# Performance work log

Hardware: AMD Instinct MI355X
Metric: run time of the kernel (lower is better)

Reference implementation:

```python
import jax, jax.numpy as jnp
import numpy as np

WEIGHT_BITS = 8
INPUT_BITS = 8


def fake_quant(t, bits):
    """Per-tensor symmetric absmax fake quantization with straight-through estimator."""
    qmax = 2.0 ** (bits - 1) - 1.0  # e.g. 127 for 8 bits
    scale = jnp.maximum(jnp.max(jnp.abs(t)), 1e-8) / qmax
    q = jnp.round(t / scale) * scale
    return t + jax.lax.stop_gradient(q - t)


def setup_inputs() -> dict:
    key = jax.random.key(0)
    k0, k1, k2, k3 = jax.random.split(key, 4)
    d, f, n = 4096, 11008, 4096
    s_in = 1.0 / np.sqrt(d)
    s_ff = 1.0 / np.sqrt(f)
    return {
        "x": jax.random.normal(k0, (n, d), jnp.float32),
        "w1": jax.random.normal(k1, (f, d), jnp.float32) * s_in,  # fc1: embed -> ffn
        "w3": jax.random.normal(k2, (f, d), jnp.float32) * s_in,  # fc3: gate proj
        "w2": jax.random.normal(k3, (d, f), jnp.float32) * s_ff,  # fc2: ffn -> embed
    }


def reference(x, w1, w3, w2):
    # quantized fc3 -> silu gate
    xq = fake_quant(x, INPUT_BITS)
    gate = jax.nn.silu(jnp.einsum('nd,fd->nf', xq, fake_quant(w3, WEIGHT_BITS)))
    # quantized fc1, multiplied by gate (GLU)
    h = jnp.einsum('nd,fd->nf', xq, fake_quant(w1, WEIGHT_BITS)) * gate
    # subln=False -> no ffn_layernorm; dropout=0 (eval)
    hq = fake_quant(h, INPUT_BITS)
    out = jnp.einsum('nf,df->nd', hq, fake_quant(w2, WEIGHT_BITS))
    return out
```

## Files before the change

### kernel.cpp

```cpp
#include <hip/hip_runtime.h>
#include <hip/hip_bf16.h>

typedef __attribute__((ext_vector_type(4))) int int4v;

#define MFMA_I8(a, b, c) __builtin_amdgcn_mfma_i32_16x16x64_i8((a), (b), (c), 0, 0, 0)
#define GLDS16(g, l)                                                                        \
  __builtin_amdgcn_global_load_lds((const __attribute__((address_space(1))) void*)(g),      \
                                   (__attribute__((address_space(3))) void*)(l), 16, 0, 0)
#define SBAR() __builtin_amdgcn_s_barrier()
#define SCHED0() __builtin_amdgcn_sched_barrier(0)

static constexpr int NTOK = 4096;
static constexpr int DDIM = 4096;
static constexpr int FDIM = 11008;


__device__ __forceinline__ float wave_max64(float m) {
#pragma unroll
  for (int o = 32; o > 0; o >>= 1) m = fmaxf(m, __shfl_xor(m, o));
  return m;
}

__global__ void zero_slots(unsigned* s) {
  if (threadIdx.x < 16) s[threadIdx.x] = 0u;
}

__device__ __forceinline__ void absmax_body(const float* __restrict__ p, int n4,
                                            unsigned* __restrict__ slot) {
  float m = 0.f;
  const int stride = gridDim.x * blockDim.x;
  for (int i = blockIdx.x * blockDim.x + threadIdx.x; i < n4; i += stride) {
    float4 v = reinterpret_cast<const float4*>(p)[i];
    m = fmaxf(fmaxf(fabsf(v.x), fabsf(v.y)), fmaxf(fmaxf(fabsf(v.z), fabsf(v.w)), m));
  }
  m = wave_max64(m);
  __shared__ float wm[4];
  const int lane = threadIdx.x & 63, w = threadIdx.x >> 6;
  if (lane == 0) wm[w] = m;
  __syncthreads();
  if (threadIdx.x == 0) {
    m = fmaxf(fmaxf(wm[0], wm[1]), fmaxf(wm[2], wm[3]));
    atomicMax(slot, __float_as_uint(m));
  }
}

__global__ void absmax4(const float* x, const float* w1, const float* w3, const float* w2,
                        unsigned* slots, int n4x, int n4w) {
  const int seg = blockIdx.y;
  const float* p = (seg == 0) ? x : (seg == 1) ? w1 : (seg == 2) ? w3 : w2;
  absmax_body(p, seg == 0 ? n4x : n4w, slots + seg);
}

__device__ __forceinline__ void quant_body(const float* __restrict__ in,
                                           unsigned* __restrict__ out, int n4,
                                           const unsigned* __restrict__ slot) {
  const float s = fmaxf(__uint_as_float(*slot), 1e-8f) / 127.0f;
  const int stride = gridDim.x * blockDim.x;
  for (int i = blockIdx.x * blockDim.x + threadIdx.x; i < n4; i += stride) {
    float4 v = reinterpret_cast<const float4*>(in)[i];
    const int q0 = (int)rintf(v.x / s), q1 = (int)rintf(v.y / s);
    const int q2 = (int)rintf(v.z / s), q3 = (int)rintf(v.w / s);
    out[i] = (unsigned)(q0 & 255) | ((unsigned)(q1 & 255) << 8) |
             ((unsigned)(q2 & 255) << 16) | ((unsigned)(q3 & 255) << 24);
  }
}

__device__ __forceinline__ void quantW_frag_body(const float* __restrict__ in,
                                                 int4v* __restrict__ out,
                                                 const unsigned* __restrict__ slot,
                                                 int K, int NKT, int total) {
  const float s = fmaxf(__uint_as_float(*slot), 1e-8f) / 127.0f;
  const int stride = gridDim.x * blockDim.x;
  for (int u = blockIdx.x * blockDim.x + threadIdx.x; u < total; u += stride) {
    const int block = u >> 8;
    const int sidx = u & 255;
    const int fi = sidx >> 6;
    const int l = sidx & 63;
    const int p = block / NKT;
    const int kt = block - p * NKT;
    const int row = p * 32 + (fi & 1) * 16 + (l & 15);
    const int k0 = kt * 128 + (fi >> 1) * 64 + (l >> 4) * 16;
    const float4* src = reinterpret_cast<const float4*>(in + (size_t)row * K + k0);
    unsigned r[4];
#pragma unroll
    for (int j = 0; j < 4; ++j) {
      float4 v = src[j];
      const int q0 = (int)rintf(v.x / s), q1 = (int)rintf(v.y / s);
      const int q2 = (int)rintf(v.z / s), q3 = (int)rintf(v.w / s);
      r[j] = (unsigned)(q0 & 255) | ((unsigned)(q1 & 255) << 8) |
             ((unsigned)(q2 & 255) << 16) | ((unsigned)(q3 & 255) << 24);
    }
    out[u] = (int4v){(int)r[0], (int)r[1], (int)r[2], (int)r[3]};
  }
}

__global__ void quant4(const float* x, const float* w1, const float* w3, const float* w2,
                       unsigned* qx, unsigned* qw1, unsigned* qw3, unsigned* qw2,
                       const unsigned* slots, int n4x, int n4w) {
  const int seg = blockIdx.y;
  const int totW = FDIM * (DDIM / 16);
  if (seg == 0) quant_body(x, qx, n4x, slots + 0);
  else if (seg == 1) quantW_frag_body(w1, (int4v*)qw1, slots + 1, DDIM, DDIM / 128, totW);
  else if (seg == 2) quantW_frag_body(w3, (int4v*)qw3, slots + 2, DDIM, DDIM / 128, totW);
  else quant_body(w2, qw2, n4w, slots + 3);
}

__global__ void quant_kernel(const float* __restrict__ in, unsigned* __restrict__ out,
                             int n4, const unsigned* __restrict__ slot) {
  quant_body(in, out, n4, slot);
}

__global__ __launch_bounds__(256, 2) void gemm_glu(
    const signed char* __restrict__ Aq, const signed char* __restrict__ B3f,
    const signed char* __restrict__ B1f, float* __restrict__ H,
    const unsigned* __restrict__ slots, unsigned* __restrict__ hslot) {
  constexpr int K = DDIM;
  constexpr int NT = K >> 7;
  __shared__ char lds[32768];

  const int t = threadIdx.x;
  const int l = t & 63;
  const int w = t >> 6;

  const int gx = gridDim.x, gy = gridDim.y;
  const int nwg = gx * gy;
  const int i0 = blockIdx.y * gx + blockIdx.x;
  const int cid = (i0 & 7) * (nwg >> 3) + (i0 >> 3);
  const int rowA0 = (cid % gy) << 7;
  const int colB0 = (cid / gy) << 7;

  const int rlA = t >> 3;
  const int glA = (t & 7) ^ (rlA & 7);
  const signed char* aP = Aq + (size_t)(rowA0 + rlA) * K + glA * 16;
  const size_t r32 = (size_t)32 * K;
  const int stW = w * 1024;

  const int p0 = (colB0 >> 5) + w;
  const signed char* w3b = B3f + (size_t)p0 * 32 * 4096 + l * 16;
  const signed char* w1b = B1f + (size_t)p0 * 32 * 4096 + l * 16;

#define STAGE_A(KT, BUF)                                   \
  do {                                                     \
    const size_t kO_ = (size_t)(KT) * 128;                 \
    GLDS16(aP + kO_, &lds[(BUF) + stW]);                   \
    GLDS16(aP + r32 + kO_, &lds[(BUF) + 4096 + stW]);      \
    GLDS16(aP + 2 * r32 + kO_, &lds[(BUF) + 8192 + stW]);  \
    GLDS16(aP + 3 * r32 + kO_, &lds[(BUF) + 12288 + stW]); \
  } while (0)

#define LDSF(BASE, R, G)                                                      \
  (*reinterpret_cast<const int4v*>(                                           \
      &lds[(BASE) + (R)*128 + (((G) ^ ((R)&7)) << 4)]))

  int4v acc3[8][2], acc1[8][2];
#pragma unroll
  for (int m = 0; m < 8; ++m)
#pragma unroll
    for (int n = 0; n < 2; ++n) {
      acc3[m][n] = (int4v){0, 0, 0, 0};
      acc1[m][n] = (int4v){0, 0, 0, 0};
    }

  const int lr = l & 15;
  const int cr = l >> 4;

  int4v b3k0[2], b3k1[2], b1k0[2], b1k1[2];

  STAGE_A(0, 0);
  {
    b3k0[0] = *(const int4v*)(w3b);
    b3k0[1] = *(const int4v*)(w3b + 1024);
    b3k1[0] = *(const int4v*)(w3b + 2048);
    b3k1[1] = *(const int4v*)(w3b + 3072);
    b1k0[0] = *(const int4v*)(w1b);
    b1k0[1] = *(const int4v*)(w1b + 1024);
    b1k1[0] = *(const int4v*)(w1b + 2048);
    b1k1[1] = *(const int4v*)(w1b + 3072);
  }

  for (int kt = 0; kt < NT; ++kt) {
    const int rb = (kt & 1) * 16384;
    const bool nx = (kt + 1 < NT);
    const signed char* p3n = w3b + (size_t)(kt + 1) * 4096;
    const signed char* p1n = w1b + (size_t)(kt + 1) * 4096;

    SCHED0();
    asm volatile("s_waitcnt vmcnt(8)" ::: "memory");
    SBAR();
    SCHED0();

    if (nx) STAGE_A(kt + 1, rb ^ 16384);

    int4v a_[8];
#pragma unroll
    for (int m = 0; m < 8; ++m) a_[m] = LDSF(rb, m * 16 + lr, cr);
    __builtin_amdgcn_s_setprio(1);
#pragma unroll
    for (int m = 0; m < 8; ++m) {
      acc3[m][0] = MFMA_I8(a_[m], b3k0[0], acc3[m][0]);
      acc3[m][1] = MFMA_I8(a_[m], b3k0[1], acc3[m][1]);
      acc1[m][0] = MFMA_I8(a_[m], b1k0[0], acc1[m][0]);
      acc1[m][1] = MFMA_I8(a_[m], b1k0[1], acc1[m][1]);
    }
    __builtin_amdgcn_s_setprio(0);

    if (nx) {
      b3k0[0] = *(const int4v*)(p3n);
      b3k0[1] = *(const int4v*)(p3n + 1024);
      b1k0[0] = *(const int4v*)(p1n);
      b1k0[1] = *(const int4v*)(p1n + 1024);
    }

#pragma unroll
    for (int m = 0; m < 8; ++m) a_[m] = LDSF(rb, m * 16 + lr, 4 + cr);
    __builtin_amdgcn_s_setprio(1);
#pragma unroll
    for (int m = 0; m < 8; ++m) {
      acc3[m][0] = MFMA_I8(a_[m], b3k1[0], acc3[m][0]);
      acc3[m][1] = MFMA_I8(a_[m], b3k1[1], acc3[m][1]);
      acc1[m][0] = MFMA_I8(a_[m], b1k1[0], acc1[m][0]);
      acc1[m][1] = MFMA_I8(a_[m], b1k1[1], acc1[m][1]);
    }
    __builtin_amdgcn_s_setprio(0);

    if (nx) {
      b3k1[0] = *(const int4v*)(p3n + 2048);
      b3k1[1] = *(const int4v*)(p3n + 3072);
      b1k1[0] = *(const int4v*)(p1n + 2048);
      b1k1[1] = *(const int4v*)(p1n + 3072);
    }
  }

  const float sx = fmaxf(__uint_as_float(slots[0]), 1e-8f) / 127.0f;
  const float sw1 = fmaxf(__uint_as_float(slots[1]), 1e-8f) / 127.0f;
  const float sw3 = fmaxf(__uint_as_float(slots[2]), 1e-8f) / 127.0f;
  const float s3 = sx * sw3, s1 = sx * sw1;
  const int crow0 = rowA0 + ((l >> 4) << 2);
  const int ccol0 = colB0 + w * 32 + lr;
  float hmax = 0.f;
#pragma unroll
  for (int m = 0; m < 8; ++m)
#pragma unroll
    for (int n = 0; n < 2; ++n)
#pragma unroll
      for (int j = 0; j < 4; ++j) {
        const int row = crow0 + m * 16 + j;
        const int col = ccol0 + n * 16;
        const float g = (float)acc3[m][n][j] * s3;
        const float gate = g / (1.f + expf(-g));
        const float h = (float)acc1[m][n][j] * s1 * gate;
        H[(size_t)row * FDIM + col] = h;
        hmax = fmaxf(hmax, fabsf(h));
      }
  hmax = wave_max64(hmax);
  if (l == 0) atomicMax(hslot, __float_as_uint(hmax));
#undef STAGE_A
#undef LDSF
}

__global__ __launch_bounds__(512, 2) void gemm_down(
    const signed char* __restrict__ Aq, const signed char* __restrict__ Bq,
    float* __restrict__ C, const unsigned* __restrict__ slots, int sA, int sB,
    int K, int ldc) {
  __shared__ char lds[131072];

  const int t = threadIdx.x;
  const int l = t & 63;
  const int w = t >> 6;
  const int wm = w >> 2;
  const int wn = w & 3;

  const int gx = gridDim.x, gy = gridDim.y;
  const int nwg = gx * gy;
  const int i0 = blockIdx.y * gx + blockIdx.x;
  const int cid = (i0 & 7) * (nwg >> 3) + (i0 >> 3);
  const int rowA0 = (cid % gy) << 8;
  const int colB0 = (cid / gy) << 8;

  const int rl = t >> 3;
  const int gl = (t & 7) ^ (rl & 7);
  const signed char* aP = Aq + (size_t)(rowA0 + rl) * K + gl * 16;
  const signed char* bP = Bq + (size_t)(colB0 + rl) * K + gl * 16;
  const size_t r64 = (size_t)64 * K;
  const int stW = w * 1024;

#define STAGE8(KO, BASE)                                             \
  do {                                                               \
    GLDS16(aP + (KO), &lds[(BASE) + stW]);                           \
    GLDS16(aP + r64 + (KO), &lds[(BASE) + 8192 + stW]);              \
    GLDS16(aP + 2 * r64 + (KO), &lds[(BASE) + 16384 + stW]);         \
    GLDS16(aP + 3 * r64 + (KO), &lds[(BASE) + 24576 + stW]);         \
    GLDS16(bP + (KO), &lds[(BASE) + 32768 + stW]);                   \
    GLDS16(bP + r64 + (KO), &lds[(BASE) + 40960 + stW]);             \
    GLDS16(bP + 2 * r64 + (KO), &lds[(BASE) + 49152 + stW]);         \
    GLDS16(bP + 3 * r64 + (KO), &lds[(BASE) + 57344 + stW]);         \
  } while (0)

#define LDSF(BASE, ROW, G)                                                    \
  (*reinterpret_cast<const int4v*>(                                           \
      &lds[(BASE) + (ROW)*128 + (((G) ^ ((ROW)&7)) << 4)]))

  int4v acc[8][4];
#pragma unroll
  for (int m = 0; m < 8; ++m)
#pragma unroll
    for (int n = 0; n < 4; ++n) acc[m][n] = (int4v){0, 0, 0, 0};

  const int NT = K >> 7;
  const int arow = wm * 128 + (l & 15);
  const int brow = wn * 64 + (l & 15);
  const int cr = l >> 4;

  STAGE8(0, 0);

  for (int kt = 0; kt < NT; ++kt) {
    const int rb = (kt & 1) * 65536;
    SCHED0();
    asm volatile("s_waitcnt vmcnt(0)" ::: "memory");
    SBAR();
    SCHED0();

    if (kt + 1 < NT) STAGE8((size_t)(kt + 1) * 128, rb ^ 65536);

#pragma unroll
    for (int kk = 0; kk < 2; ++kk) {
      int4v a[8], b[4];
#pragma unroll
      for (int m = 0; m < 8; ++m) a[m] = LDSF(rb, arow + m * 16, kk * 4 + cr);
#pragma unroll
      for (int n = 0; n < 4; ++n) b[n] = LDSF(rb + 32768, brow + n * 16, kk * 4 + cr);
      __builtin_amdgcn_s_setprio(1);
#pragma unroll
      for (int m = 0; m < 8; ++m)
#pragma unroll
        for (int n = 0; n < 4; ++n) acc[m][n] = MFMA_I8(a[m], b[n], acc[m][n]);
      __builtin_amdgcn_s_setprio(0);
    }
  }

  const float sa = fmaxf(__uint_as_float(slots[sA]), 1e-8f) / 127.0f;
  const float sb2 = fmaxf(__uint_as_float(slots[sB]), 1e-8f) / 127.0f;
  const float s = sa * sb2;
  const int crow0 = rowA0 + wm * 128 + ((l >> 4) << 2);
  const int ccol0 = colB0 + wn * 64 + (l & 15);
#pragma unroll
  for (int m = 0; m < 8; ++m)
#pragma unroll
    for (int n = 0; n < 4; ++n)
#pragma unroll
      for (int j = 0; j < 4; ++j) {
        const int row = crow0 + m * 16 + j;
        const int col = ccol0 + n * 16;
        C[(size_t)row * ldc + col] = (float)acc[m][n][j] * s;
      }
#undef STAGE8
#undef LDSF
}


extern "C" void kernel_launch(void* const* d_in, const int* in_sizes, int n_in,
                              void* d_out, int out_size, void* d_ws, size_t ws_size,
                              hipStream_t stream) {
  const float* x = (const float*)d_in[0];
  const float* w1 = (const float*)d_in[1];
  const float* w3 = (const float*)d_in[2];
  const float* w2 = (const float*)d_in[3];
  float* out = (float*)d_out;
  char* ws = (char*)d_ws;

  unsigned* slots = (unsigned*)ws;
  size_t off = 256;
  signed char* qx = (signed char*)(ws + off);
  off += (size_t)NTOK * DDIM;
  signed char* qw3 = (signed char*)(ws + off);
  off += (size_t)FDIM * DDIM;
  signed char* qw1 = (signed char*)(ws + off);
  off += (size_t)FDIM * DDIM;
  signed char* qw2 = (signed char*)(ws + off);
  off += (size_t)FDIM * DDIM;
  float* H = (float*)(ws + off);
  off += (size_t)NTOK * FDIM * 4;
  signed char* qh = (signed char*)(ws + off);
  off += (size_t)NTOK * FDIM;

  const int n4x = NTOK * DDIM / 4;
  const int n4w = FDIM * DDIM / 4;
  const int n4h = NTOK * FDIM / 4;

  zero_slots<<<1, 64, 0, stream>>>(slots);
  absmax4<<<dim3(512, 4), 256, 0, stream>>>(x, w1, w3, w2, slots, n4x, n4w);
  quant4<<<dim3(2048, 4), 256, 0, stream>>>(x, w1, w3, w2, (unsigned*)qx, (unsigned*)qw1,
                                            (unsigned*)qw3, (unsigned*)qw2, slots, n4x, n4w);

  const dim3 gGlu(FDIM / 128, NTOK / 128);
  gemm_glu<<<gGlu, 256, 0, stream>>>(qx, qw3, qw1, H, slots, slots + 4);
  quant_kernel<<<2048, 256, 0, stream>>>(H, (unsigned*)qh, n4h, slots + 4);
  const dim3 gDn(DDIM / 256, NTOK / 256);
  gemm_down<<<gDn, 512, 0, stream>>>(qh, qw2, out, slots, 4, 3, FDIM, DDIM);
}
```

Before: 819.0 us.

## Double K-tile depth in GLU GEMM and replace slot-zero kernel with memset

The GLU GEMM now stages 256-wide K tiles of A into a 64KB double-buffered LDS (previously 128-wide in 32KB). It prefetches four k-steps of B fragments into registers and processes the M dimension in two halves, which halves the number of barriers and loop iterations. This adds LDS usage that may cut the two-blocks-per-CU occupancy and raises register pressure from the larger B prefetch. The zero_slots launch is also replaced by hipMemsetAsync.

```diff
diff --git a/kernel.cpp b/kernel.cpp
--- a/kernel.cpp
+++ b/kernel.cpp
@@ -19,10 +19,6 @@
 #pragma unroll
   for (int o = 32; o > 0; o >>= 1) m = fmaxf(m, __shfl_xor(m, o));
   return m;
-}
-
-__global__ void zero_slots(unsigned* s) {
-  if (threadIdx.x < 16) s[threadIdx.x] = 0u;
 }
 
 __device__ __forceinline__ void absmax_body(const float* __restrict__ p, int n4,
@@ -115,8 +111,8 @@
     const signed char* __restrict__ B1f, float* __restrict__ H,
     const unsigned* __restrict__ slots, unsigned* __restrict__ hslot) {
   constexpr int K = DDIM;
-  constexpr int NT = K >> 7;
-  __shared__ char lds[32768];
+  constexpr int NT = K >> 8;
+  __shared__ char lds[65536];
 
   const int t = threadIdx.x;
   const int l = t & 63;
@@ -129,28 +125,32 @@
   const int rowA0 = (cid % gy) << 7;
   const int colB0 = (cid / gy) << 7;
 
-  const int rlA = t >> 3;
-  const int glA = (t & 7) ^ (rlA & 7);
+  const int rlA = t >> 4;
+  const int glA = (t & 15) ^ (rlA & 7);
   const signed char* aP = Aq + (size_t)(rowA0 + rlA) * K + glA * 16;
-  const size_t r32 = (size_t)32 * K;
+  const size_t r16 = (size_t)16 * K;
   const int stW = w * 1024;
 
   const int p0 = (colB0 >> 5) + w;
   const signed char* w3b = B3f + (size_t)p0 * 32 * 4096 + l * 16;
   const signed char* w1b = B1f + (size_t)p0 * 32 * 4096 + l * 16;
 
-#define STAGE_A(KT, BUF)                                   \
-  do {                                                     \
-    const size_t kO_ = (size_t)(KT) * 128;                 \
-    GLDS16(aP + kO_, &lds[(BUF) + stW]);                   \
-    GLDS16(aP + r32 + kO_, &lds[(BUF) + 4096 + stW]);      \
-    GLDS16(aP + 2 * r32 + kO_, &lds[(BUF) + 8192 + stW]);  \
-    GLDS16(aP + 3 * r32 + kO_, &lds[(BUF) + 12288 + stW]); \
+#define STAGE_A(KT, BUF)                                              \
+  do {                                                                \
+    const size_t kO_ = (size_t)(KT) * 256;                            \
+    GLDS16(aP + kO_, &lds[(BUF) + stW]);                              \
+    GLDS16(aP + r16 + kO_, &lds[(BUF) + 4096 + stW]);                 \
+    GLDS16(aP + 2 * r16 + kO_, &lds[(BUF) + 8192 + stW]);             \
+    GLDS16(aP + 3 * r16 + kO_, &lds[(BUF) + 12288 + stW]);            \
+    GLDS16(aP + 4 * r16 + kO_, &lds[(BUF) + 16384 + stW]);            \
+    GLDS16(aP + 5 * r16 + kO_, &lds[(BUF) + 20480 + stW]);            \
+    GLDS16(aP + 6 * r16 + kO_, &lds[(BUF) + 24576 + stW]);            \
+    GLDS16(aP + 7 * r16 + kO_, &lds[(BUF) + 28672 + stW]);            \
   } while (0)
 
 #define LDSF(BASE, R, G)                                                      \
   (*reinterpret_cast<const int4v*>(                                           \
-      &lds[(BASE) + (R)*128 + (((G) ^ ((R)&7)) << 4)]))
+      &lds[(BASE) + (R)*256 + (((G) ^ ((R)&7)) << 4)]))
 
   int4v acc3[8][2], acc1[8][2];
 #pragma unroll
@@ -164,70 +164,60 @@
   const int lr = l & 15;
   const int cr = l >> 4;
 
-  int4v b3k0[2], b3k1[2], b1k0[2], b1k1[2];
+  int4v b3s[4][2], b1s[4][2];
 
   STAGE_A(0, 0);
-  {
-    b3k0[0] = *(const int4v*)(w3b);
-    b3k0[1] = *(const int4v*)(w3b + 1024);
-    b3k1[0] = *(const int4v*)(w3b + 2048);
-    b3k1[1] = *(const int4v*)(w3b + 3072);
-    b1k0[0] = *(const int4v*)(w1b);
-    b1k0[1] = *(const int4v*)(w1b + 1024);
-    b1k1[0] = *(const int4v*)(w1b + 2048);
-    b1k1[1] = *(const int4v*)(w1b + 3072);
+#pragma unroll
+  for (int kk = 0; kk < 4; ++kk) {
+    const size_t o_ = (size_t)(kk >> 1) * 4096 + (size_t)(kk & 1) * 2048;
+    b3s[kk][0] = *(const int4v*)(w3b + o_);
+    b3s[kk][1] = *(const int4v*)(w3b + o_ + 1024);
+    b1s[kk][0] = *(const int4v*)(w1b + o_);
+    b1s[kk][1] = *(const int4v*)(w1b + o_ + 1024);
   }
 
   for (int kt = 0; kt < NT; ++kt) {
-    const int rb = (kt & 1) * 16384;
+    const int rb = (kt & 1) * 32768;
     const bool nx = (kt + 1 < NT);
-    const signed char* p3n = w3b + (size_t)(kt + 1) * 4096;
-    const signed char* p1n = w1b + (size_t)(kt + 1) * 4096;
 
     SCHED0();
-    asm volatile("s_waitcnt vmcnt(8)" ::: "memory");
+    if (nx) {
+      asm volatile("s_waitcnt vmcnt(16)" ::: "memory");
+    } else {
+      asm volatile("s_waitcnt vmcnt(0)" ::: "memory");
+    }
     SBAR();
     SCHED0();
 
-    if (nx) STAGE_A(kt + 1, rb ^ 16384);
-
-    int4v a_[8];
-#pragma unroll
-    for (int m = 0; m < 8; ++m) a_[m] = LDSF(rb, m * 16 + lr, cr);
-    __builtin_amdgcn_s_setprio(1);
-#pragma unroll
-    for (int m = 0; m < 8; ++m) {
-      acc3[m][0] = MFMA_I8(a_[m], b3k0[0], acc3[m][0]);
-      acc3[m][1] = MFMA_I8(a_[m], b3k0[1], acc3[m][1]);
-      acc1[m][0] = MFMA_I8(a_[m], b1k0[0], acc1[m][0]);
-      acc1[m][1] = MFMA_I8(a_[m], b1k0[1], acc1[m][1]);
-    }
-    __builtin_amdgcn_s_setprio(0);
-
-    if (nx) {
-      b3k0[0] = *(const int4v*)(p3n);
-      b3k0[1] = *(const int4v*)(p3n + 1024);
-      b1k0[0] = *(const int4v*)(p1n);
-      b1k0[1] = *(const int4v*)(p1n + 1024);
-    }
-
-#pragma unroll
-    for (int m = 0; m < 8; ++m) a_[m] = LDSF(rb, m * 16 + lr, 4 + cr);
-    __builtin_amdgcn_s_setprio(1);
-#pragma unroll
-    for (int m = 0; m < 8; ++m) {
-      acc3[m][0] = MFMA_I8(a_[m], b3k1[0], acc3[m][0]);
-      acc3[m][1] = MFMA_I8(a_[m], b3k1[1], acc3[m][1]);
-      acc1[m][0] = MFMA_I8(a_[m], b1k1[0], acc1[m][0]);
-      acc1[m][1] = MFMA_I8(a_[m], b1k1[1], acc1[m][1]);
-    }
-    __builtin_amdgcn_s_setprio(0);
-
-    if (nx) {
-      b3k1[0] = *(const int4v*)(p3n + 2048);
-      b3k1[1] = *(const int4v*)(p3n + 3072);
-      b1k1[0] = *(const int4v*)(p1n + 2048);
-      b1k1[1] = *(const int4v*)(p1n + 3072);
+    if (nx) STAGE_A(kt + 1, rb ^ 32768);
+
+#pragma unroll
+    for (int kk = 0; kk < 4; ++kk) {
+#pragma unroll
+      for (int mh = 0; mh < 2; ++mh) {
+        int4v a_[4];
+#pragma unroll
+        for (int m = 0; m < 4; ++m)
+          a_[m] = LDSF(rb, (mh * 4 + m) * 16 + lr, kk * 4 + cr);
+        __builtin_amdgcn_s_setprio(1);
+#pragma unroll
+        for (int m = 0; m < 4; ++m) {
+          const int mi = mh * 4 + m;
+          acc3[mi][0] = MFMA_I8(a_[m], b3s[kk][0], acc3[mi][0]);
+          acc3[mi][1] = MFMA_I8(a_[m], b3s[kk][1], acc3[mi][1]);
+          acc1[mi][0] = MFMA_I8(a_[m], b1s[kk][0], acc1[mi][0]);
+          acc1[mi][1] = MFMA_I8(a_[m], b1s[kk][1], acc1[mi][1]);
+        }
+        __builtin_amdgcn_s_setprio(0);
+      }
+      if (nx) {
+        const size_t o_ = (size_t)(2 * (kt + 1) + (kk >> 1)) * 4096 +
+                          (size_t)(kk & 1) * 2048;
+        b3s[kk][0] = *(const int4v*)(w3b + o_);
+        b3s[kk][1] = *(const int4v*)(w3b + o_ + 1024);
+        b1s[kk][0] = *(const int4v*)(w1b + o_);
+        b1s[kk][1] = *(const int4v*)(w1b + o_ + 1024);
+      }
     }
   }
 
@@ -387,7 +377,7 @@
   const int n4w = FDIM * DDIM / 4;
   const int n4h = NTOK * FDIM / 4;
 
-  zero_slots<<<1, 64, 0, stream>>>(slots);
+  hipMemsetAsync(slots, 0, 64, stream);
   absmax4<<<dim3(512, 4), 256, 0, stream>>>(x, w1, w3, w2, slots, n4x, n4w);
   quant4<<<dim3(2048, 4), 256, 0, stream>>>(x, w1, w3, w2, (unsigned*)qx, (unsigned*)qw1,
                                             (unsigned*)qw3, (unsigned*)qw2, slots, n4x, n4w);
```

New measurement: 814.6 us. About the same (-0.5%).
